# Performance work log

Hardware: AMD Instinct MI355X
Metric: run time of the kernel (lower is better)

The kernel has to match this reference:

```python
import jax, jax.numpy as jnp
import numpy as np

N_NODES = 100000
N_EDGES = 1600000
D_IN = 128
D_OUT = 128


def setup_inputs() -> dict:
    key = jax.random.key(0)
    k1, k2, k3 = jax.random.split(key, 3)
    x = jax.random.normal(k1, (N_NODES, D_IN), dtype=jnp.float32)
    edge_index = jax.random.randint(k2, (2, N_EDGES), 0, N_NODES, dtype=jnp.int64)
    # Glorot-style init for the GCN weight, zero bias (PyG defaults)
    W = jax.random.normal(k3, (D_IN, D_OUT), dtype=jnp.float32) * (1.0 / np.sqrt(D_IN))
    b = jnp.zeros((D_OUT,), dtype=jnp.float32)
    return {"x": x, "edge_index": edge_index, "W": W, "b": b}


def reference(x, edge_index, W, b):
    # GCNConv (PyG defaults: add_self_loops=True, normalize=True):
    #   out = D^{-1/2} (A + I) D^{-1/2} (X W) + b
    # Dropout is identity in eval mode.
    n = x.shape[0]
    loop = jnp.arange(n, dtype=edge_index.dtype)
    src = jnp.concatenate([edge_index[0], loop])  # [E + N]
    dst = jnp.concatenate([edge_index[1], loop])  # [E + N]

    h = x @ W  # [N, D_OUT] -- transform before aggregation (fewer FLOPs if D_OUT <= D_IN)

    # Degree of each node counting self-loops, computed over targets.
    ones = jnp.ones(dst.shape[0], dtype=h.dtype)
    deg = jax.ops.segment_sum(ones, dst, num_segments=n)  # [N]
    deg_inv_sqrt = jnp.where(deg > 0, jax.lax.rsqrt(deg), 0.0)

    # Symmetric normalization per edge: d_src^{-1/2} * d_dst^{-1/2}
    norm = deg_inv_sqrt[src] * deg_inv_sqrt[dst]  # [E + N]

    # Gather messages, scale, scatter-add to targets.
    msgs = h[src] * norm[:, None]  # [E + N, D_OUT]
    out = jax.ops.segment_sum(msgs, dst, num_segments=n)  # [N, D_OUT]
    return out + b
```

## Files before the change

kernel.cpp:

```cpp
#include <hip/hip_runtime.h>

#define DD 128
#define CAP 12288

typedef __attribute__((ext_vector_type(8))) short bf16x8;
typedef __attribute__((ext_vector_type(4))) float f32x4;

__device__ inline unsigned short f2b(float f) {
    unsigned int u = __float_as_uint(f);
    u += 0x7fffu + ((u >> 16) & 1u);
    return (unsigned short)(u >> 16);
}

__device__ inline void bacc(float4& a, uint2 v) {
    a.x += __uint_as_float(v.x << 16);
    a.y += __uint_as_float(v.x & 0xffff0000u);
    a.z += __uint_as_float(v.y << 16);
    a.w += __uint_as_float(v.y & 0xffff0000u);
}

__device__ inline void bacc16(float4& a, float4& b, uint4 v) {
    a.x += __uint_as_float(v.x << 16);
    a.y += __uint_as_float(v.x & 0xffff0000u);
    a.z += __uint_as_float(v.y << 16);
    a.w += __uint_as_float(v.y & 0xffff0000u);
    b.x += __uint_as_float(v.z << 16);
    b.y += __uint_as_float(v.z & 0xffff0000u);
    b.z += __uint_as_float(v.w << 16);
    b.w += __uint_as_float(v.w & 0xffff0000u);
}

__global__ void k_init(int* __restrict__ cur, int nbuck) {
    int b = blockIdx.x * 256 + threadIdx.x;
    if (b < nbuck) cur[b] = b * CAP;
}

__global__ __launch_bounds__(256) void k_binA(const int* __restrict__ src,
                                              const int* __restrict__ dst, int E,
                                              int chunk, int nbuck,
                                              int* __restrict__ cur,
                                              int* __restrict__ binned) {
    __shared__ int hist[256];
    __shared__ int base[256];
    __shared__ int curs[256];
    const int t = threadIdx.x;
    const int e0 = blockIdx.x * chunk;
    const int e1 = min(e0 + chunk, E);

    if (t < 256) { hist[t] = 0; curs[t] = 0; }
    __syncthreads();
    for (int e = e0 + t; e < e1; e += 256)
        atomicAdd(&hist[dst[e] >> 9], 1);
    __syncthreads();
    if (t < nbuck && hist[t] > 0)
        base[t] = atomicAdd(&cur[t], hist[t]);
    __syncthreads();
    for (int e = e0 + t; e < e1; e += 256) {
        int d = dst[e];
        int b = d >> 9;
        int p = atomicAdd(&curs[b], 1);
        int idx = base[b] + p;
        if (idx < (b + 1) * CAP)
            binned[idx] = (src[e] << 9) | (d & 511);
    }
}

__global__ __launch_bounds__(512) void k_binB(int* __restrict__ binned,
                                              const int* __restrict__ cur,
                                              int* __restrict__ off,
                                              int* __restrict__ cnt,
                                              float* __restrict__ dinv,
                                              int n) {
    __shared__ int hist[512];
    __shared__ int curs[512];
    __shared__ int sorted[CAP];
    const int t = threadIdx.x;
    const int b = blockIdx.x;
    const int base = b * CAP;
    const int cb = cur[b] - base;

    hist[t] = 0;
    __syncthreads();
    for (int i = t; i < cb; i += 512)
        atomicAdd(&hist[binned[base + i] & 511], 1);
    __syncthreads();
    int v = hist[t];
    for (int st = 1; st < 512; st <<= 1) {
        int tv = (t >= st) ? hist[t - st] : 0;
        __syncthreads();
        hist[t] += tv;
        __syncthreads();
    }
    int excl = hist[t] - v;
    curs[t] = excl;
    int d = b * 512 + t;
    if (d < n) {
        off[d]  = base + excl;
        cnt[d]  = v;
        dinv[d] = rsqrtf((float)v + 1.0f);
    }
    __syncthreads();
    for (int i = t; i < cb; i += 512) {
        int pk = binned[base + i];
        int p = atomicAdd(&curs[pk & 511], 1);
        sorted[p] = pk >> 9;
    }
    __syncthreads();
    for (int i = t; i < cb; i += 512)
        binned[base + i] = sorted[i];
}

__global__ __launch_bounds__(256) void k_wt(const float* __restrict__ W,
                                            unsigned short* __restrict__ Wt) {
    int idx = blockIdx.x * 256 + threadIdx.x;
    int k = idx >> 7, c = idx & 127;
    Wt[c * DD + k] = f2b(W[k * DD + c]);
}

__global__ __launch_bounds__(256) void k_gemm(const float* __restrict__ x,
                                              const unsigned short* __restrict__ Wt,
                                              const float* __restrict__ dinv,
                                              unsigned short* __restrict__ hs,
                                              int n) {
    const int t = threadIdx.x;
    const int wave = t >> 6, lane = t & 63;
    const int rowbase = blockIdx.x * 256 + wave * 64;
    const int l15 = lane & 15, l4 = lane >> 4;

    bf16x8 a[4][4];
    #pragma unroll
    for (int rb = 0; rb < 4; ++rb) {
        int r = rowbase + rb * 16 + l15;
        int rc = min(r, n - 1);
        const float* xr = x + (size_t)rc * DD;
        #pragma unroll
        for (int kc = 0; kc < 4; ++kc) {
            int k0 = kc * 32 + l4 * 8;
            float4 f0 = *(const float4*)(xr + k0);
            float4 f1 = *(const float4*)(xr + k0 + 4);
            bf16x8 fr;
            fr[0] = (short)f2b(f0.x); fr[1] = (short)f2b(f0.y);
            fr[2] = (short)f2b(f0.z); fr[3] = (short)f2b(f0.w);
            fr[4] = (short)f2b(f1.x); fr[5] = (short)f2b(f1.y);
            fr[6] = (short)f2b(f1.z); fr[7] = (short)f2b(f1.w);
            a[rb][kc] = fr;
        }
    }

    float dv[4][4];
    #pragma unroll
    for (int rb = 0; rb < 4; ++rb)
        #pragma unroll
        for (int vv = 0; vv < 4; ++vv) {
            int r = rowbase + rb * 16 + l4 * 4 + vv;
            dv[rb][vv] = dinv[min(r, n - 1)];
        }

    #pragma unroll
    for (int cb = 0; cb < 8; ++cb) {
        int c0 = cb * 16;
        f32x4 acc[4] = {};
        #pragma unroll
        for (int kc = 0; kc < 4; ++kc) {
            bf16x8 bfrag = *(const bf16x8*)(Wt + (size_t)(c0 + l15) * DD + kc * 32 + l4 * 8);
            #pragma unroll
            for (int rb = 0; rb < 4; ++rb)
                acc[rb] = __builtin_amdgcn_mfma_f32_16x16x32_bf16(a[rb][kc], bfrag, acc[rb], 0, 0, 0);
        }
        #pragma unroll
        for (int rb = 0; rb < 4; ++rb) {
            int r0 = rowbase + rb * 16 + l4 * 4;
            #pragma unroll
            for (int vv = 0; vv < 4; ++vv) {
                int r = r0 + vv;
                if (r < n)
                    hs[(size_t)r * DD + c0 + l15] = f2b(acc[rb][vv] * dv[rb][vv]);
            }
        }
    }
}

__global__ __launch_bounds__(256, 8) void k_agg(const uint4* __restrict__ hsr,
                                                const int* __restrict__ ssrc,
                                                const int* __restrict__ off,
                                                const int* __restrict__ cnt,
                                                const float* __restrict__ dinv,
                                                const float* __restrict__ bias,
                                                float* __restrict__ out, int n) {
    const int t = threadIdx.x;
    const int wave = t >> 6, lane = t & 63;
    const int q  = lane >> 4;
    const int ql = lane & 15;
    const int d = blockIdx.x * 4 + wave;
    if (d >= n) return;

    const int s0 = off[d];
    const int c  = cnt[d];

    float4 accA = {0.f, 0.f, 0.f, 0.f};
    float4 accB = {0.f, 0.f, 0.f, 0.f};

    uint4 vself = hsr[(size_t)d * 16 + ql];

    int idx[6];
    #pragma unroll
    for (int r = 0; r < 6; ++r) {
        int e = r * 4 + q;
        idx[r] = ssrc[s0 + ((e < c) ? e : 0)];
    }
    #pragma unroll
    for (int r = 0; r < 6; ++r) {
        int e = r * 4 + q;
        idx[r] = (e < c) ? idx[r] : d;
    }

    uint4 val[6];
    #pragma unroll
    for (int r = 0; r < 6; ++r)
        val[r] = hsr[(size_t)idx[r] * 16 + ql];

    if (q == 0) bacc16(accA, accB, vself);
    #pragma unroll
    for (int r = 0; r < 6; ++r) {
        int e = r * 4 + q;
        if (e < c) bacc16(accA, accB, val[r]);
    }

    for (int i = 24 + q; i < c; i += 4) {
        int s = ssrc[s0 + i];
        uint4 v = hsr[(size_t)s * 16 + ql];
        bacc16(accA, accB, v);
    }

    #pragma unroll
    for (int m = 16; m <= 32; m <<= 1) {
        accA.x += __shfl_xor(accA.x, m);
        accA.y += __shfl_xor(accA.y, m);
        accA.z += __shfl_xor(accA.z, m);
        accA.w += __shfl_xor(accA.w, m);
        accB.x += __shfl_xor(accB.x, m);
        accB.y += __shfl_xor(accB.y, m);
        accB.z += __shfl_xor(accB.z, m);
        accB.w += __shfl_xor(accB.w, m);
    }

    if (q == 0) {
        float di = dinv[d];
        float4 b0 = ((const float4*)bias)[ql * 2];
        float4 b1 = ((const float4*)bias)[ql * 2 + 1];
        float4 o0, o1;
        o0.x = accA.x * di + b0.x;
        o0.y = accA.y * di + b0.y;
        o0.z = accA.z * di + b0.z;
        o0.w = accA.w * di + b0.w;
        o1.x = accB.x * di + b1.x;
        o1.y = accB.y * di + b1.y;
        o1.z = accB.z * di + b1.z;
        o1.w = accB.w * di + b1.w;
        float4* orow = (float4*)(out + (size_t)d * DD);
        orow[ql * 2]     = o0;
        orow[ql * 2 + 1] = o1;
    }
}

extern "C" void kernel_launch(void* const* d_in, const int* in_sizes, int n_in,
                              void* d_out, int out_size, void* d_ws, size_t ws_size,
                              hipStream_t stream) {
    const float* x  = (const float*)d_in[0];
    const int*   ei = (const int*)d_in[1];
    const float* W  = (const float*)d_in[2];
    const float* b  = (const float*)d_in[3];
    float* out = (float*)d_out;

    const int n = in_sizes[0] / DD;
    const int E = in_sizes[1] / 2;
    const int* src = ei;
    const int* dst = ei + E;

    const int nbuck = (n + 511) >> 9;

    unsigned short* hs = (unsigned short*)d_ws;
    unsigned short* Wt = hs + (size_t)n * DD;
    int*   binned = (int*)(Wt + DD * DD);
    int*   off    = binned + (size_t)nbuck * CAP;
    int*   cnt    = off + n;
    float* dinv   = (float*)(cnt + n);
    int*   cur    = (int*)(dinv + n);

    const int nblkA = 1024;
    const int chunk = (E + nblkA - 1) / nblkA;

    k_init<<<(nbuck + 255) / 256, 256, 0, stream>>>(cur, nbuck);
    k_binA<<<nblkA, 256, 0, stream>>>(src, dst, E, chunk, nbuck, cur, binned);
    k_binB<<<nbuck, 512, 0, stream>>>(binned, cur, off, cnt, dinv, n);
    k_wt  <<<DD * DD / 256, 256, 0, stream>>>(W, Wt);
    k_gemm<<<(n + 255) / 256, 256, 0, stream>>>(x, Wt, dinv, hs, n);
    k_agg <<<(n + 3) / 4, 256, 0, stream>>>((const uint4*)hs, binned, off, cnt,
                                            dinv, b, out, n);
}
```

Before: 136.9 us.

## Map one destination node per quarter-wave with software-pipelined batched gathers

The aggregation kernel now gives each 16-lane quarter-wave its own destination node instead of splitting one node's edges across the four quarters of a wave. This removes the cross-quarter shuffle reduction, and the grid shrinks to a quarter of the blocks. Up to 24 neighbor rows are loaded in three batches of eight, with sched_barriers placed so index loads for the next batch overlap accumulation of the previous one. The gathers use more registers, so launch bounds drop from 8 to 5 blocks per CU. Since degrees vary per node, lanes within a wave now diverge more in the tail loop.

After: 139.7 us. +2.1%, slower.

```diff
diff --git a/kernel.cpp b/kernel.cpp
--- a/kernel.cpp
+++ b/kernel.cpp
@@ -10,13 +10,6 @@
     unsigned int u = __float_as_uint(f);
     u += 0x7fffu + ((u >> 16) & 1u);
     return (unsigned short)(u >> 16);
-}
-
-__device__ inline void bacc(float4& a, uint2 v) {
-    a.x += __uint_as_float(v.x << 16);
-    a.y += __uint_as_float(v.x & 0xffff0000u);
-    a.z += __uint_as_float(v.y << 16);
-    a.w += __uint_as_float(v.y & 0xffff0000u);
 }
 
 __device__ inline void bacc16(float4& a, float4& b, uint4 v) {
@@ -180,7 +173,7 @@
     }
 }
 
-__global__ __launch_bounds__(256, 8) void k_agg(const uint4* __restrict__ hsr,
+__global__ __launch_bounds__(256, 5) void k_agg(const uint4* __restrict__ hsr,
                                                 const int* __restrict__ ssrc,
                                                 const int* __restrict__ off,
                                                 const int* __restrict__ cnt,
@@ -191,60 +184,72 @@
     const int wave = t >> 6, lane = t & 63;
     const int q  = lane >> 4;
     const int ql = lane & 15;
-    const int d = blockIdx.x * 4 + wave;
-    if (d >= n) return;
-
-    const int s0 = off[d];
-    const int c  = cnt[d];
+    const int d = blockIdx.x * 16 + wave * 4 + q;
+    const bool alive = (d < n);
+    const int dc = alive ? d : (n - 1);
+
+    const int s0 = off[dc];
+    const int c  = alive ? cnt[dc] : 0;
+
+    uint4 vself = hsr[(size_t)dc * 16 + ql];
 
     float4 accA = {0.f, 0.f, 0.f, 0.f};
     float4 accB = {0.f, 0.f, 0.f, 0.f};
 
-    uint4 vself = hsr[(size_t)d * 16 + ql];
-
-    int idx[6];
-    #pragma unroll
-    for (int r = 0; r < 6; ++r) {
-        int e = r * 4 + q;
-        idx[r] = ssrc[s0 + ((e < c) ? e : 0)];
-    }
-    #pragma unroll
-    for (int r = 0; r < 6; ++r) {
-        int e = r * 4 + q;
-        idx[r] = (e < c) ? idx[r] : d;
-    }
-
-    uint4 val[6];
-    #pragma unroll
-    for (int r = 0; r < 6; ++r)
-        val[r] = hsr[(size_t)idx[r] * 16 + ql];
-
-    if (q == 0) bacc16(accA, accB, vself);
-    #pragma unroll
-    for (int r = 0; r < 6; ++r) {
-        int e = r * 4 + q;
-        if (e < c) bacc16(accA, accB, val[r]);
-    }
-
-    for (int i = 24 + q; i < c; i += 4) {
+    int ia[8], ib[8], ic[8];
+    uint4 va[8], vb[8], vc[8];
+
+    #pragma unroll
+    for (int r = 0; r < 8; ++r)
+        ia[r] = ssrc[s0 + ((r < c) ? r : 0)];
+    #pragma unroll
+    for (int r = 0; r < 8; ++r)
+        ia[r] = (r < c) ? ia[r] : dc;
+    #pragma unroll
+    for (int r = 0; r < 8; ++r)
+        va[r] = hsr[(size_t)ia[r] * 16 + ql];
+    #pragma unroll
+    for (int r = 0; r < 8; ++r)
+        ib[r] = ssrc[s0 + ((8 + r < c) ? 8 + r : 0)];
+    __builtin_amdgcn_sched_barrier(0);
+
+    bacc16(accA, accB, vself);
+    #pragma unroll
+    for (int r = 0; r < 8; ++r)
+        ib[r] = (8 + r < c) ? ib[r] : dc;
+    #pragma unroll
+    for (int r = 0; r < 8; ++r)
+        vb[r] = hsr[(size_t)ib[r] * 16 + ql];
+    #pragma unroll
+    for (int r = 0; r < 8; ++r)
+        ic[r] = ssrc[s0 + ((16 + r < c) ? 16 + r : 0)];
+    __builtin_amdgcn_sched_barrier(0);
+
+    #pragma unroll
+    for (int r = 0; r < 8; ++r)
+        if (r < c) bacc16(accA, accB, va[r]);
+    #pragma unroll
+    for (int r = 0; r < 8; ++r)
+        ic[r] = (16 + r < c) ? ic[r] : dc;
+    #pragma unroll
+    for (int r = 0; r < 8; ++r)
+        vc[r] = hsr[(size_t)ic[r] * 16 + ql];
+    __builtin_amdgcn_sched_barrier(0);
+
+    #pragma unroll
+    for (int r = 0; r < 8; ++r)
+        if (8 + r < c) bacc16(accA, accB, vb[r]);
+    #pragma unroll
+    for (int r = 0; r < 8; ++r)
+        if (16 + r < c) bacc16(accA, accB, vc[r]);
+
+    for (int i = 24; i < c; ++i) {
         int s = ssrc[s0 + i];
         uint4 v = hsr[(size_t)s * 16 + ql];
         bacc16(accA, accB, v);
     }
 
-    #pragma unroll
-    for (int m = 16; m <= 32; m <<= 1) {
-        accA.x += __shfl_xor(accA.x, m);
-        accA.y += __shfl_xor(accA.y, m);
-        accA.z += __shfl_xor(accA.z, m);
-        accA.w += __shfl_xor(accA.w, m);
-        accB.x += __shfl_xor(accB.x, m);
-        accB.y += __shfl_xor(accB.y, m);
-        accB.z += __shfl_xor(accB.z, m);
-        accB.w += __shfl_xor(accB.w, m);
-    }
-
-    if (q == 0) {
+    if (alive) {
         float di = dinv[d];
         float4 b0 = ((const float4*)bias)[ql * 2];
         float4 b1 = ((const float4*)bias)[ql * 2 + 1];
@@ -295,6 +300,6 @@
     k_binB<<<nbuck, 512, 0, stream>>>(binned, cur, off, cnt, dinv, n);
     k_wt  <<<DD * DD / 256, 256, 0, stream>>>(W, Wt);
     k_gemm<<<(n + 255) / 256, 256, 0, stream>>>(x, Wt, dinv, hs, n);
-    k_agg <<<(n + 3) / 4, 256, 0, stream>>>((const uint4*)hs, binned, off, cnt,
-                                            dinv, b, out, n);
-}
+    k_agg <<<(n + 15) / 16, 256, 0, stream>>>((const uint4*)hs, binned, off, cnt,
+                                              dinv, b, out, n);
+}
```

## Halve bucket size, merge init kernels, and shrink GEMM rows per block

Applied to the files above, without the earlier changes.

Destination buckets shrink from 512 to 256 nodes, with capacity halved. This gives the k_binB sort twice as many blocks and half the shared-memory footprint per block, which should improve occupancy. The weight-transpose kernel and the cursor-init kernel are merged into one launch, removing a launch. The GEMM now handles 16 rows per wave instead of 64, giving four times as many blocks and fewer live registers, at the cost of reloading W fragments more often. Because capacity is halved, a bucket that overflows its 6144 slots would silently drop edges.

New measurement: 153.0 us. 11.8% more time.

```diff
diff --git a/kernel.cpp b/kernel.cpp
--- a/kernel.cpp
+++ b/kernel.cpp
@@ -1,7 +1,7 @@
 #include <hip/hip_runtime.h>
 
 #define DD 128
-#define CAP 12288
+#define CAP 6144
 
 typedef __attribute__((ext_vector_type(8))) short bf16x8;
 typedef __attribute__((ext_vector_type(4))) float f32x4;
@@ -10,13 +10,6 @@
     unsigned int u = __float_as_uint(f);
     u += 0x7fffu + ((u >> 16) & 1u);
     return (unsigned short)(u >> 16);
-}
-
-__device__ inline void bacc(float4& a, uint2 v) {
-    a.x += __uint_as_float(v.x << 16);
-    a.y += __uint_as_float(v.x & 0xffff0000u);
-    a.z += __uint_as_float(v.y << 16);
-    a.w += __uint_as_float(v.y & 0xffff0000u);
 }
 
 __device__ inline void bacc16(float4& a, float4& b, uint4 v) {
@@ -30,9 +23,18 @@
     b.w += __uint_as_float(v.w & 0xffff0000u);
 }
 
-__global__ void k_init(int* __restrict__ cur, int nbuck) {
-    int b = blockIdx.x * 256 + threadIdx.x;
-    if (b < nbuck) cur[b] = b * CAP;
+__global__ __launch_bounds__(256) void k_pre(const float* __restrict__ W,
+                                             unsigned short* __restrict__ Wt,
+                                             int* __restrict__ cur, int nbuck) {
+    int bid = blockIdx.x;
+    if (bid < 64) {
+        int idx = bid * 256 + threadIdx.x;
+        int k = idx >> 7, c = idx & 127;
+        Wt[c * DD + k] = f2b(W[k * DD + c]);
+    } else {
+        int b = (bid - 64) * 256 + threadIdx.x;
+        if (b < nbuck) cur[b] = b * CAP;
+    }
 }
 
 __global__ __launch_bounds__(256) void k_binA(const int* __restrict__ src,
@@ -40,28 +42,29 @@
                                               int chunk, int nbuck,
                                               int* __restrict__ cur,
                                               int* __restrict__ binned) {
-    __shared__ int hist[256];
-    __shared__ int base[256];
-    __shared__ int curs[256];
+    __shared__ int hist[512];
+    __shared__ int base[512];
+    __shared__ int curs[512];
     const int t = threadIdx.x;
     const int e0 = blockIdx.x * chunk;
     const int e1 = min(e0 + chunk, E);
 
-    if (t < 256) { hist[t] = 0; curs[t] = 0; }
+    for (int b = t; b < 512; b += 256) { hist[b] = 0; curs[b] = 0; }
     __syncthreads();
     for (int e = e0 + t; e < e1; e += 256)
-        atomicAdd(&hist[dst[e] >> 9], 1);
-    __syncthreads();
-    if (t < nbuck && hist[t] > 0)
-        base[t] = atomicAdd(&cur[t], hist[t]);
+        atomicAdd(&hist[dst[e] >> 8], 1);
+    __syncthreads();
+    for (int b = t; b < nbuck; b += 256)
+        if (hist[b] > 0)
+            base[b] = atomicAdd(&cur[b], hist[b]);
     __syncthreads();
     for (int e = e0 + t; e < e1; e += 256) {
         int d = dst[e];
-        int b = d >> 9;
+        int b = d >> 8;
         int p = atomicAdd(&curs[b], 1);
         int idx = base[b] + p;
         if (idx < (b + 1) * CAP)
-            binned[idx] = (src[e] << 9) | (d & 511);
+            binned[idx] = (src[e] << 8) | (d & 255);
     }
 }
 
@@ -71,50 +74,45 @@
                                               int* __restrict__ cnt,
                                               float* __restrict__ dinv,
                                               int n) {
-    __shared__ int hist[512];
-    __shared__ int curs[512];
+    __shared__ int hist[256];
+    __shared__ int curs[256];
     __shared__ int sorted[CAP];
     const int t = threadIdx.x;
     const int b = blockIdx.x;
     const int base = b * CAP;
     const int cb = cur[b] - base;
 
-    hist[t] = 0;
+    if (t < 256) hist[t] = 0;
     __syncthreads();
     for (int i = t; i < cb; i += 512)
-        atomicAdd(&hist[binned[base + i] & 511], 1);
-    __syncthreads();
-    int v = hist[t];
-    for (int st = 1; st < 512; st <<= 1) {
-        int tv = (t >= st) ? hist[t - st] : 0;
+        atomicAdd(&hist[binned[base + i] & 255], 1);
+    __syncthreads();
+    int v = (t < 256) ? hist[t] : 0;
+    for (int st = 1; st < 256; st <<= 1) {
+        int tv = (t >= st && t < 256) ? hist[t - st] : 0;
         __syncthreads();
-        hist[t] += tv;
+        if (t < 256) hist[t] += tv;
         __syncthreads();
     }
-    int excl = hist[t] - v;
-    curs[t] = excl;
-    int d = b * 512 + t;
-    if (d < n) {
-        off[d]  = base + excl;
-        cnt[d]  = v;
-        dinv[d] = rsqrtf((float)v + 1.0f);
+    if (t < 256) {
+        int excl = hist[t] - v;
+        curs[t] = excl;
+        int d = b * 256 + t;
+        if (d < n) {
+            off[d]  = base + excl;
+            cnt[d]  = v;
+            dinv[d] = rsqrtf((float)v + 1.0f);
+        }
     }
     __syncthreads();
     for (int i = t; i < cb; i += 512) {
         int pk = binned[base + i];
-        int p = atomicAdd(&curs[pk & 511], 1);
-        sorted[p] = pk >> 9;
+        int p = atomicAdd(&curs[pk & 255], 1);
+        sorted[p] = pk >> 8;
     }
     __syncthreads();
     for (int i = t; i < cb; i += 512)
         binned[base + i] = sorted[i];
-}
-
-__global__ __launch_bounds__(256) void k_wt(const float* __restrict__ W,
-                                            unsigned short* __restrict__ Wt) {
-    int idx = blockIdx.x * 256 + threadIdx.x;
-    int k = idx >> 7, c = idx & 127;
-    Wt[c * DD + k] = f2b(W[k * DD + c]);
 }
 
 __global__ __launch_bounds__(256) void k_gemm(const float* __restrict__ x,
@@ -124,58 +122,48 @@
                                               int n) {
     const int t = threadIdx.x;
     const int wave = t >> 6, lane = t & 63;
-    const int rowbase = blockIdx.x * 256 + wave * 64;
+    const int rowbase = blockIdx.x * 64 + wave * 16;
     const int l15 = lane & 15, l4 = lane >> 4;
 
-    bf16x8 a[4][4];
-    #pragma unroll
-    for (int rb = 0; rb < 4; ++rb) {
-        int r = rowbase + rb * 16 + l15;
-        int rc = min(r, n - 1);
-        const float* xr = x + (size_t)rc * DD;
-        #pragma unroll
-        for (int kc = 0; kc < 4; ++kc) {
-            int k0 = kc * 32 + l4 * 8;
-            float4 f0 = *(const float4*)(xr + k0);
-            float4 f1 = *(const float4*)(xr + k0 + 4);
-            bf16x8 fr;
-            fr[0] = (short)f2b(f0.x); fr[1] = (short)f2b(f0.y);
-            fr[2] = (short)f2b(f0.z); fr[3] = (short)f2b(f0.w);
-            fr[4] = (short)f2b(f1.x); fr[5] = (short)f2b(f1.y);
-            fr[6] = (short)f2b(f1.z); fr[7] = (short)f2b(f1.w);
-            a[rb][kc] = fr;
-        }
-    }
-
-    float dv[4][4];
-    #pragma unroll
-    for (int rb = 0; rb < 4; ++rb)
-        #pragma unroll
-        for (int vv = 0; vv < 4; ++vv) {
-            int r = rowbase + rb * 16 + l4 * 4 + vv;
-            dv[rb][vv] = dinv[min(r, n - 1)];
-        }
+    const int r = rowbase + l15;
+    const int rc = min(r, n - 1);
+    const float* xr = x + (size_t)rc * DD;
+
+    bf16x8 a[4];
+    #pragma unroll
+    for (int kc = 0; kc < 4; ++kc) {
+        int k0 = kc * 32 + l4 * 8;
+        float4 f0 = *(const float4*)(xr + k0);
+        float4 f1 = *(const float4*)(xr + k0 + 4);
+        bf16x8 fr;
+        fr[0] = (short)f2b(f0.x); fr[1] = (short)f2b(f0.y);
+        fr[2] = (short)f2b(f0.z); fr[3] = (short)f2b(f0.w);
+        fr[4] = (short)f2b(f1.x); fr[5] = (short)f2b(f1.y);
+        fr[6] = (short)f2b(f1.z); fr[7] = (short)f2b(f1.w);
+        a[kc] = fr;
+    }
+
+    float dv[4];
+    #pragma unroll
+    for (int vv = 0; vv < 4; ++vv) {
+        int r2 = rowbase + l4 * 4 + vv;
+        dv[vv] = dinv[min(r2, n - 1)];
+    }
 
     #pragma unroll
     for (int cb = 0; cb < 8; ++cb) {
         int c0 = cb * 16;
-        f32x4 acc[4] = {};
+        f32x4 acc = {};
         #pragma unroll
         for (int kc = 0; kc < 4; ++kc) {
             bf16x8 bfrag = *(const bf16x8*)(Wt + (size_t)(c0 + l15) * DD + kc * 32 + l4 * 8);
-            #pragma unroll
-            for (int rb = 0; rb < 4; ++rb)
-                acc[rb] = __builtin_amdgcn_mfma_f32_16x16x32_bf16(a[rb][kc], bfrag, acc[rb], 0, 0, 0);
+            acc = __builtin_amdgcn_mfma_f32_16x16x32_bf16(a[kc], bfrag, acc, 0, 0, 0);
         }
         #pragma unroll
-        for (int rb = 0; rb < 4; ++rb) {
-            int r0 = rowbase + rb * 16 + l4 * 4;
-            #pragma unroll
-            for (int vv = 0; vv < 4; ++vv) {
-                int r = r0 + vv;
-                if (r < n)
-                    hs[(size_t)r * DD + c0 + l15] = f2b(acc[rb][vv] * dv[rb][vv]);
-            }
+        for (int vv = 0; vv < 4; ++vv) {
+            int r3 = rowbase + l4 * 4 + vv;
+            if (r3 < n)
+                hs[(size_t)r3 * DD + c0 + l15] = f2b(acc[vv] * dv[vv]);
         }
     }
 }
@@ -277,7 +265,7 @@
     const int* src = ei;
     const int* dst = ei + E;
 
-    const int nbuck = (n + 511) >> 9;
+    const int nbuck = (n + 255) >> 8;
 
     unsigned short* hs = (unsigned short*)d_ws;
     unsigned short* Wt = hs + (size_t)n * DD;
@@ -290,11 +278,10 @@
     const int nblkA = 1024;
     const int chunk = (E + nblkA - 1) / nblkA;
 
-    k_init<<<(nbuck + 255) / 256, 256, 0, stream>>>(cur, nbuck);
+    k_pre <<<64 + (nbuck + 255) / 256, 256, 0, stream>>>(W, Wt, cur, nbuck);
     k_binA<<<nblkA, 256, 0, stream>>>(src, dst, E, chunk, nbuck, cur, binned);
     k_binB<<<nbuck, 512, 0, stream>>>(binned, cur, off, cnt, dinv, n);
-    k_wt  <<<DD * DD / 256, 256, 0, stream>>>(W, Wt);
-    k_gemm<<<(n + 255) / 256, 256, 0, stream>>>(x, Wt, dinv, hs, n);
+    k_gemm<<<(n + 63) / 64, 256, 0, stream>>>(x, Wt, dinv, hs, n);
     k_agg <<<(n + 3) / 4, 256, 0, stream>>>((const uint4*)hs, binned, off, cnt,
                                             dinv, b, out, n);
 }
```

## Run GEMM concurrently with bucket sort and move src-degree scaling into aggregation

Applied to the files above, without the earlier changes.

The GEMM no longer depends on dinv: the source-side normalization is applied per edge in the aggregation kernel, which loads dinv[src] for each gathered row. This lets the bucket-sort stage and the GEMM run as one fused launch with disjoint block roles, so they overlap. The Wt transpose and cursor init also merge into one launch. The cost is an extra per-edge dinv gather plus multiplies in k_agg, and GEMM blocks now carry 512 threads and a large shared-memory reservation that can limit occupancy.

Result: no change. 134.5 us (-1.7%).

```diff
diff --git a/kernel.cpp b/kernel.cpp
--- a/kernel.cpp
+++ b/kernel.cpp
@@ -12,27 +12,29 @@
     return (unsigned short)(u >> 16);
 }
 
-__device__ inline void bacc(float4& a, uint2 v) {
-    a.x += __uint_as_float(v.x << 16);
-    a.y += __uint_as_float(v.x & 0xffff0000u);
-    a.z += __uint_as_float(v.y << 16);
-    a.w += __uint_as_float(v.y & 0xffff0000u);
-}
-
-__device__ inline void bacc16(float4& a, float4& b, uint4 v) {
-    a.x += __uint_as_float(v.x << 16);
-    a.y += __uint_as_float(v.x & 0xffff0000u);
-    a.z += __uint_as_float(v.y << 16);
-    a.w += __uint_as_float(v.y & 0xffff0000u);
-    b.x += __uint_as_float(v.z << 16);
-    b.y += __uint_as_float(v.z & 0xffff0000u);
-    b.z += __uint_as_float(v.w << 16);
-    b.w += __uint_as_float(v.w & 0xffff0000u);
-}
-
-__global__ void k_init(int* __restrict__ cur, int nbuck) {
-    int b = blockIdx.x * 256 + threadIdx.x;
-    if (b < nbuck) cur[b] = b * CAP;
+__device__ inline void bacc16f(float4& a, float4& b, uint4 v, float s) {
+    a.x += __uint_as_float(v.x << 16) * s;
+    a.y += __uint_as_float(v.x & 0xffff0000u) * s;
+    a.z += __uint_as_float(v.y << 16) * s;
+    a.w += __uint_as_float(v.y & 0xffff0000u) * s;
+    b.x += __uint_as_float(v.z << 16) * s;
+    b.y += __uint_as_float(v.z & 0xffff0000u) * s;
+    b.z += __uint_as_float(v.w << 16) * s;
+    b.w += __uint_as_float(v.w & 0xffff0000u) * s;
+}
+
+__global__ __launch_bounds__(256) void k_pre(const float* __restrict__ W,
+                                             unsigned short* __restrict__ Wt,
+                                             int* __restrict__ cur, int nbuck) {
+    int bid = blockIdx.x;
+    if (bid < 64) {
+        int idx = bid * 256 + threadIdx.x;
+        int k = idx >> 7, c = idx & 127;
+        Wt[c * DD + k] = f2b(W[k * DD + c]);
+    } else {
+        int b = (bid - 64) * 256 + threadIdx.x;
+        if (b < nbuck) cur[b] = b * CAP;
+    }
 }
 
 __global__ __launch_bounds__(256) void k_binA(const int* __restrict__ src,
@@ -65,116 +67,100 @@
     }
 }
 
-__global__ __launch_bounds__(512) void k_binB(int* __restrict__ binned,
+__global__ __launch_bounds__(512) void k_fuse(int* __restrict__ binned,
                                               const int* __restrict__ cur,
                                               int* __restrict__ off,
                                               int* __restrict__ cnt,
                                               float* __restrict__ dinv,
-                                              int n) {
+                                              const float* __restrict__ x,
+                                              const unsigned short* __restrict__ Wt,
+                                              unsigned short* __restrict__ hs,
+                                              int n, int nbuck) {
     __shared__ int hist[512];
     __shared__ int curs[512];
     __shared__ int sorted[CAP];
     const int t = threadIdx.x;
-    const int b = blockIdx.x;
-    const int base = b * CAP;
-    const int cb = cur[b] - base;
-
-    hist[t] = 0;
-    __syncthreads();
-    for (int i = t; i < cb; i += 512)
-        atomicAdd(&hist[binned[base + i] & 511], 1);
-    __syncthreads();
-    int v = hist[t];
-    for (int st = 1; st < 512; st <<= 1) {
-        int tv = (t >= st) ? hist[t - st] : 0;
-        __syncthreads();
-        hist[t] += tv;
-        __syncthreads();
-    }
-    int excl = hist[t] - v;
-    curs[t] = excl;
-    int d = b * 512 + t;
-    if (d < n) {
-        off[d]  = base + excl;
-        cnt[d]  = v;
-        dinv[d] = rsqrtf((float)v + 1.0f);
-    }
-    __syncthreads();
-    for (int i = t; i < cb; i += 512) {
-        int pk = binned[base + i];
-        int p = atomicAdd(&curs[pk & 511], 1);
-        sorted[p] = pk >> 9;
-    }
-    __syncthreads();
-    for (int i = t; i < cb; i += 512)
-        binned[base + i] = sorted[i];
-}
-
-__global__ __launch_bounds__(256) void k_wt(const float* __restrict__ W,
-                                            unsigned short* __restrict__ Wt) {
-    int idx = blockIdx.x * 256 + threadIdx.x;
-    int k = idx >> 7, c = idx & 127;
-    Wt[c * DD + k] = f2b(W[k * DD + c]);
-}
-
-__global__ __launch_bounds__(256) void k_gemm(const float* __restrict__ x,
-                                              const unsigned short* __restrict__ Wt,
-                                              const float* __restrict__ dinv,
-                                              unsigned short* __restrict__ hs,
-                                              int n) {
-    const int t = threadIdx.x;
-    const int wave = t >> 6, lane = t & 63;
-    const int rowbase = blockIdx.x * 256 + wave * 64;
-    const int l15 = lane & 15, l4 = lane >> 4;
-
-    bf16x8 a[4][4];
-    #pragma unroll
-    for (int rb = 0; rb < 4; ++rb) {
-        int r = rowbase + rb * 16 + l15;
-        int rc = min(r, n - 1);
-        const float* xr = x + (size_t)rc * DD;
+
+    if (blockIdx.x < (unsigned)nbuck) {
+        const int b = blockIdx.x;
+        const int base = b * CAP;
+        const int cb = cur[b] - base;
+
+        hist[t] = 0;
+        __syncthreads();
+        for (int i = t; i < cb; i += 512)
+            atomicAdd(&hist[binned[base + i] & 511], 1);
+        __syncthreads();
+        int v = hist[t];
+        for (int st = 1; st < 512; st <<= 1) {
+            int tv = (t >= st) ? hist[t - st] : 0;
+            __syncthreads();
+            hist[t] += tv;
+            __syncthreads();
+        }
+        int excl = hist[t] - v;
+        curs[t] = excl;
+        int d = b * 512 + t;
+        if (d < n) {
+            off[d]  = base + excl;
+            cnt[d]  = v;
+            dinv[d] = rsqrtf((float)v + 1.0f);
+        }
+        __syncthreads();
+        for (int i = t; i < cb; i += 512) {
+            int pk = binned[base + i];
+            int p = atomicAdd(&curs[pk & 511], 1);
+            sorted[p] = pk >> 9;
+        }
+        __syncthreads();
+        for (int i = t; i < cb; i += 512)
+            binned[base + i] = sorted[i];
+    } else {
+        const int gb = blockIdx.x - nbuck;
+        const int wave = t >> 6, lane = t & 63;
+        const int rowbase = gb * 256 + wave * 32;
+        const int l15 = lane & 15, l4 = lane >> 4;
+
+        bf16x8 a[2][4];
         #pragma unroll
-        for (int kc = 0; kc < 4; ++kc) {
-            int k0 = kc * 32 + l4 * 8;
-            float4 f0 = *(const float4*)(xr + k0);
-            float4 f1 = *(const float4*)(xr + k0 + 4);
-            bf16x8 fr;
-            fr[0] = (short)f2b(f0.x); fr[1] = (short)f2b(f0.y);
-            fr[2] = (short)f2b(f0.z); fr[3] = (short)f2b(f0.w);
-            fr[4] = (short)f2b(f1.x); fr[5] = (short)f2b(f1.y);
-            fr[6] = (short)f2b(f1.z); fr[7] = (short)f2b(f1.w);
-            a[rb][kc] = fr;
-        }
-    }
-
-    float dv[4][4];
-    #pragma unroll
-    for (int rb = 0; rb < 4; ++rb)
+        for (int rb = 0; rb < 2; ++rb) {
+            int r = rowbase + rb * 16 + l15;
+            int rc = min(r, n - 1);
+            const float* xr = x + (size_t)rc * DD;
+            #pragma unroll
+            for (int kc = 0; kc < 4; ++kc) {
+                int k0 = kc * 32 + l4 * 8;
+                float4 f0 = *(const float4*)(xr + k0);
+                float4 f1 = *(const float4*)(xr + k0 + 4);
+                bf16x8 fr;
+                fr[0] = (short)f2b(f0.x); fr[1] = (short)f2b(f0.y);
+                fr[2] = (short)f2b(f0.z); fr[3] = (short)f2b(f0.w);
+                fr[4] = (short)f2b(f1.x); fr[5] = (short)f2b(f1.y);
+                fr[6] = (short)f2b(f1.z); fr[7] = (short)f2b(f1.w);
+                a[rb][kc] = fr;
+            }
+        }
+
         #pragma unroll
-        for (int vv = 0; vv < 4; ++vv) {
-            int r = rowbase + rb * 16 + l4 * 4 + vv;
-            dv[rb][vv] = dinv[min(r, n - 1)];
-        }
-
-    #pragma unroll
-    for (int cb = 0; cb < 8; ++cb) {
-        int c0 = cb * 16;
-        f32x4 acc[4] = {};
-        #pragma unroll
-        for (int kc = 0; kc < 4; ++kc) {
-            bf16x8 bfrag = *(const bf16x8*)(Wt + (size_t)(c0 + l15) * DD + kc * 32 + l4 * 8);
+        for (int cb8 = 0; cb8 < 8; ++cb8) {
+            int c0 = cb8 * 16;
+            f32x4 acc[2] = {};
             #pragma unroll
-            for (int rb = 0; rb < 4; ++rb)
-                acc[rb] = __builtin_amdgcn_mfma_f32_16x16x32_bf16(a[rb][kc], bfrag, acc[rb], 0, 0, 0);
-        }
-        #pragma unroll
-        for (int rb = 0; rb < 4; ++rb) {
-            int r0 = rowbase + rb * 16 + l4 * 4;
+            for (int kc = 0; kc < 4; ++kc) {
+                bf16x8 bfrag = *(const bf16x8*)(Wt + (size_t)(c0 + l15) * DD + kc * 32 + l4 * 8);
+                #pragma unroll
+                for (int rb = 0; rb < 2; ++rb)
+                    acc[rb] = __builtin_amdgcn_mfma_f32_16x16x32_bf16(a[rb][kc], bfrag, acc[rb], 0, 0, 0);
+            }
             #pragma unroll
-            for (int vv = 0; vv < 4; ++vv) {
-                int r = r0 + vv;
-                if (r < n)
-                    hs[(size_t)r * DD + c0 + l15] = f2b(acc[rb][vv] * dv[rb][vv]);
+            for (int rb = 0; rb < 2; ++rb) {
+                int r0 = rowbase + rb * 16 + l4 * 4;
+                #pragma unroll
+                for (int vv = 0; vv < 4; ++vv) {
+                    int r = r0 + vv;
+                    if (r < n)
+                        hs[(size_t)r * DD + c0 + l15] = f2b(acc[rb][vv]);
+                }
             }
         }
     }
@@ -196,6 +182,7 @@
 
     const int s0 = off[d];
     const int c  = cnt[d];
+    const float di = dinv[d];
 
     float4 accA = {0.f, 0.f, 0.f, 0.f};
     float4 accB = {0.f, 0.f, 0.f, 0.f};
@@ -215,21 +202,24 @@
     }
 
     uint4 val[6];
-    #pragma unroll
-    for (int r = 0; r < 6; ++r)
+    float sc[6];
+    #pragma unroll
+    for (int r = 0; r < 6; ++r) {
         val[r] = hsr[(size_t)idx[r] * 16 + ql];
-
-    if (q == 0) bacc16(accA, accB, vself);
+        sc[r]  = dinv[idx[r]];
+    }
+
+    if (q == 0) bacc16f(accA, accB, vself, di);
     #pragma unroll
     for (int r = 0; r < 6; ++r) {
         int e = r * 4 + q;
-        if (e < c) bacc16(accA, accB, val[r]);
+        if (e < c) bacc16f(accA, accB, val[r], sc[r]);
     }
 
     for (int i = 24 + q; i < c; i += 4) {
         int s = ssrc[s0 + i];
         uint4 v = hsr[(size_t)s * 16 + ql];
-        bacc16(accA, accB, v);
+        bacc16f(accA, accB, v, dinv[s]);
     }
 
     #pragma unroll
@@ -245,7 +235,6 @@
     }
 
     if (q == 0) {
-        float di = dinv[d];
         float4 b0 = ((const float4*)bias)[ql * 2];
         float4 b1 = ((const float4*)bias)[ql * 2 + 1];
         float4 o0, o1;
@@ -290,11 +279,12 @@
     const int nblkA = 1024;
     const int chunk = (E + nblkA - 1) / nblkA;
 
-    k_init<<<(nbuck + 255) / 256, 256, 0, stream>>>(cur, nbuck);
+    const int ngemm = (n + 255) / 256;
+
+    k_pre <<<64 + (nbuck + 255) / 256, 256, 0, stream>>>(W, Wt, cur, nbuck);
     k_binA<<<nblkA, 256, 0, stream>>>(src, dst, E, chunk, nbuck, cur, binned);
-    k_binB<<<nbuck, 512, 0, stream>>>(binned, cur, off, cnt, dinv, n);
-    k_wt  <<<DD * DD / 256, 256, 0, stream>>>(W, Wt);
-    k_gemm<<<(n + 255) / 256, 256, 0, stream>>>(x, Wt, dinv, hs, n);
+    k_fuse<<<nbuck + ngemm, 512, 0, stream>>>(binned, cur, off, cnt, dinv,
+                                              x, Wt, hs, n, nbuck);
     k_agg <<<(n + 3) / 4, 256, 0, stream>>>((const uint4*)hs, binned, off, cnt,
                                             dinv, b, out, n);
 }
```
